# Optimization experiments

Measured on AMD Instinct MI355X. Metric: run time of the kernel, lower is better.

The kernel has to match this reference:

```python
import math
import jax, jax.numpy as jnp
import numpy as np

B, N, D = 32, 1025, 768        # batch, tokens (incl. CLS), backbone channels
C, CD, TD = 64, 128, 256       # num_clusters, cluster_dim, token_dim
REG = 0.1
SINKHORN_ITERS = 5


def setup_inputs() -> dict:
    key = jax.random.key(0)
    ks = jax.random.split(key, 9)
    inv = 1.0 / math.sqrt(D)
    return {
        "x": jax.random.normal(ks[0], (B, N, D), dtype=jnp.float32),
        "Wf": jax.random.normal(ks[1], (D, CD), dtype=jnp.float32) * inv,
        "bf": jnp.zeros((CD,), dtype=jnp.float32),
        "Ws": jax.random.normal(ks[2], (D, C), dtype=jnp.float32) * inv,
        "bs": jnp.zeros((C,), dtype=jnp.float32),
        "Wt": jax.random.normal(ks[3], (D, TD), dtype=jnp.float32) * inv,
        "bt": jnp.zeros((TD,), dtype=jnp.float32),
        "anchors": jax.random.normal(ks[4], (C, CD), dtype=jnp.float32) * 0.1,
        "dust_bin": jnp.array(1.0, dtype=jnp.float32),
        "sharpness": jnp.array(5.0, dtype=jnp.float32),
    }


def _sinkhorn_log(log_a, log_b, M, num_iters, reg):
    # log-domain Sinkhorn: M [B, C+1, Nt], log_a [B, C+1], log_b [B, Nt]
    M = M / reg
    u = jnp.zeros_like(log_a)
    v = jnp.zeros_like(log_b)
    for _ in range(num_iters):
        u = log_a - jax.nn.logsumexp(M + v[:, None, :], axis=2)
        v = log_b - jax.nn.logsumexp(M + u[:, :, None], axis=1)
    return M + u[:, :, None] + v[:, None, :]


def reference(x, Wf, bf, Ws, bs, Wt, bt, anchors, dust_bin, sharpness):
    Bx, Nx, _ = x.shape
    n_tok = Nx - 1
    nC = anchors.shape[0]

    t_global = x[:, 0]            # [B, D]
    fi = x[:, 1:]                 # [B, Nt, D]

    f = fi @ Wf + bf              # [B, Nt, CD]
    s = jnp.einsum('bnd,dc->bcn', fi, Ws) + bs[None, :, None]  # [B, C, Nt]
    s = s * sharpness

    dust = jnp.broadcast_to(dust_bin, (Bx, 1, n_tok))
    s_aug = jnp.concatenate([s, dust], axis=1)  # [B, C+1, Nt]

    log_b = jnp.full((Bx, n_tok), -math.log(n_tok), dtype=x.dtype)
    # n_tok (1024) > nC (64): marginals with dustbin absorbing excess mass
    log_a = jnp.concatenate([
        jnp.full((Bx, nC), -math.log(n_tok), dtype=x.dtype),
        jnp.full((Bx, 1), math.log(n_tok - nC) - math.log(n_tok), dtype=x.dtype),
    ], axis=1)

    log_P = _sinkhorn_log(log_a, log_b, s_aug, SINKHORN_ITERS, REG)
    p = jnp.exp(log_P)[:, :-1, :]  # [B, C, Nt], drop dustbin row

    # sum_n p[b,c,n] * (2*f[b,n,d] - anchors[c,d])  == GEMM + rank-1 correction
    v_agg = 2.0 * jnp.einsum('bcn,bnd->bcd', p, f) \
            - p.sum(axis=2)[:, :, None] * anchors[None]  # [B, C, CD]

    v_local = v_agg.reshape(Bx, -1)   # [B, C*CD]
    v_global = t_global @ Wt + bt     # [B, TD]
    f_out = jnp.concatenate([v_global, v_local], axis=-1)
    norm = jnp.maximum(jnp.linalg.norm(f_out, axis=-1, keepdims=True), 1e-12)
    return f_out / norm
```

## Files before the change

### kernel.cpp

```cpp
#include <hip/hip_runtime.h>

typedef unsigned short u16;
typedef __attribute__((ext_vector_type(8))) short bf16x8;
typedef __attribute__((ext_vector_type(8))) short s16x8;
typedef __attribute__((ext_vector_type(4))) float f32x4;
typedef __attribute__((ext_vector_type(4))) short s16x4;

#define OUTW 8448

static __device__ __forceinline__ float bf2f(u16 u) {
    union { unsigned int i; float f; } x; x.i = ((unsigned int)u) << 16; return x.f;
}
static __device__ __forceinline__ u16 f2bf(float f) {
    union { float f; unsigned int i; } x; x.f = f;
    unsigned int lsb = (x.i >> 16) & 1u;
    return (u16)((x.i + 0x7fffu + lsb) >> 16);
}
static __device__ __forceinline__ int kswz(int r, int c) {
    return c ^ (((r ^ (r >> 3)) & 7) << 3);
}

__global__ __launch_bounds__(256) void k_pre(
    const float* __restrict__ x, const float* __restrict__ Wf, const float* __restrict__ Ws,
    const float* __restrict__ Wt, u16* __restrict__ Bp, float* __restrict__ vg)
{
    const int bid = blockIdx.x, tid = threadIdx.x;
    if (bid < 12) {
        __shared__ float Wl[64][193];
        const int t = bid;
        #pragma unroll 4
        for (int i = 0; i < 32; ++i) {
            const int idx = i * 256 + tid, r = idx >> 7, c = idx & 127;
            Wl[r][c] = Wf[(size_t)(t * 64 + r) * 128 + c];
        }
        #pragma unroll 4
        for (int i = 0; i < 16; ++i) {
            const int idx = i * 256 + tid, r = idx >> 6, c = idx & 63;
            Wl[r][128 + c] = Ws[(size_t)(t * 64 + r) * 64 + c];
        }
        __syncthreads();
        #pragma unroll
        for (int i = 0; i < 6; ++i) {
            const int ch = i * 256 + tid, c = ch >> 3, j0 = (ch & 7) << 3;
            u16 pk[8];
            #pragma unroll
            for (int j = 0; j < 8; ++j) pk[j] = f2bf(Wl[j0 + j][c]);
            *(s16x8*)&Bp[((size_t)t * 192 + c) * 64 + j0] = *(const s16x8*)pk;
        }
    } else {
        const int blk = bid - 12;
        const int kc = blk >> 5, b = blk & 31, d = tid;
        const float* xr = x + (size_t)b * (1025 * 768) + kc * 96;
        const float* wp = Wt + (size_t)kc * 96 * 256 + d;
        float acc = 0.f;
        #pragma unroll 8
        for (int k = 0; k < 96; ++k) acc += xr[k] * wp[(size_t)k * 256];
        vg[(size_t)blk * 256 + d] = acc;
    }
}

__global__ __launch_bounds__(512, 4) void k_gemm1(
    const float* __restrict__ x, const u16* __restrict__ Bp,
    const float* __restrict__ bf_, const float* __restrict__ bs_, const float* __restrict__ sharp,
    u16* __restrict__ fT, float* __restrict__ sM)
{
    __shared__ u16 Asm[2][64][72];
    const int tid  = threadIdx.x;
    const int lane = tid & 63;
    const int w    = tid >> 6;
    const int wm   = w >> 2, wn = w & 3;
    const int b    = blockIdx.x >> 4;
    const int n0   = (blockIdx.x & 15) << 6;
    const float* Abase = x + ((size_t)b * 1025 + 1 + n0) * 768;

    const int arow = tid >> 3, ak0 = (tid & 7) << 3;
    const float* aptr = Abase + (size_t)arow * 768 + ak0;
    const int fk = (lane >> 4) << 3;
    const u16* bbase = Bp + (size_t)(wn * 48 + (lane & 15)) * 64 + fk;

    f32x4 acc[2][3] = {};
    float4 pa[2];
    bf16x8 bcur[6], bnxt[6];

    pa[0] = *(const float4*)(aptr);
    pa[1] = *(const float4*)(aptr + 4);
    #pragma unroll
    for (int nt = 0; nt < 3; ++nt)
        #pragma unroll
        for (int kk = 0; kk < 2; ++kk)
            bcur[nt * 2 + kk] = *(const bf16x8*)(bbase + nt * 1024 + kk * 32);
    {
        u16 t8[8];
        t8[0] = f2bf(pa[0].x); t8[1] = f2bf(pa[0].y); t8[2] = f2bf(pa[0].z); t8[3] = f2bf(pa[0].w);
        t8[4] = f2bf(pa[1].x); t8[5] = f2bf(pa[1].y); t8[6] = f2bf(pa[1].z); t8[7] = f2bf(pa[1].w);
        *(s16x8*)&Asm[0][arow][ak0] = *(const s16x8*)t8;
    }
    pa[0] = *(const float4*)(aptr + 64);
    pa[1] = *(const float4*)(aptr + 68);
    __syncthreads();

    for (int t = 0; t < 12; ++t) {
        const int cur = t & 1;
        if (t < 11) {
            const u16* bp1 = bbase + (size_t)(t + 1) * 12288;
            #pragma unroll
            for (int nt = 0; nt < 3; ++nt)
                #pragma unroll
                for (int kk = 0; kk < 2; ++kk)
                    bnxt[nt * 2 + kk] = *(const bf16x8*)(bp1 + nt * 1024 + kk * 32);
            u16 t8[8];
            t8[0] = f2bf(pa[0].x); t8[1] = f2bf(pa[0].y); t8[2] = f2bf(pa[0].z); t8[3] = f2bf(pa[0].w);
            t8[4] = f2bf(pa[1].x); t8[5] = f2bf(pa[1].y); t8[6] = f2bf(pa[1].z); t8[7] = f2bf(pa[1].w);
            *(s16x8*)&Asm[cur ^ 1][arow][ak0] = *(const s16x8*)t8;
        }
        if (t < 10) {
            const float* ap = aptr + (size_t)(t + 2) * 64;
            pa[0] = *(const float4*)(ap);
            pa[1] = *(const float4*)(ap + 4);
        }
        #pragma unroll
        for (int kk = 0; kk < 2; ++kk) {
            bf16x8 af[2];
            af[0] = *(const bf16x8*)&Asm[cur][wm * 32 + (lane & 15)][kk * 32 + fk];
            af[1] = *(const bf16x8*)&Asm[cur][wm * 32 + 16 + (lane & 15)][kk * 32 + fk];
            #pragma unroll
            for (int nt = 0; nt < 3; ++nt) {
                acc[0][nt] = __builtin_amdgcn_mfma_f32_16x16x32_bf16(af[0], bcur[nt * 2 + kk], acc[0][nt], 0, 0, 0);
                acc[1][nt] = __builtin_amdgcn_mfma_f32_16x16x32_bf16(af[1], bcur[nt * 2 + kk], acc[1][nt], 0, 0, 0);
            }
        }
        if (t < 11) {
            #pragma unroll
            for (int i = 0; i < 6; ++i) bcur[i] = bnxt[i];
        }
        __syncthreads();
    }

    const int rbase = (lane >> 4) << 2;
    const int cl = lane & 15;
    const float sc = sharp[0] * 10.0f;
    #pragma unroll
    for (int mt = 0; mt < 2; ++mt) {
        const int nbase = n0 + wm * 32 + mt * 16 + rbase;
        #pragma unroll
        for (int nt = 0; nt < 3; ++nt) {
            const int col16 = wn * 48 + nt * 16;
            const int c = col16 + cl;
            if (col16 < 128) {
                const float bias = bf_[c];
                u16 pk[4];
                #pragma unroll
                for (int r = 0; r < 4; ++r) pk[r] = f2bf(acc[mt][nt][r] + bias);
                *(s16x4*)&fT[((size_t)b * 128 + c) * 1024 + nbase] = *(const s16x4*)pk;
            } else {
                const int cm = c - 128;
                const float bias = bs_[cm];
                float4 v;
                v.x = (acc[mt][nt][0] + bias) * sc;
                v.y = (acc[mt][nt][1] + bias) * sc;
                v.z = (acc[mt][nt][2] + bias) * sc;
                v.w = (acc[mt][nt][3] + bias) * sc;
                *(float4*)&sM[((size_t)b * 64 + cm) * 1024 + nbase] = v;
            }
        }
    }
}

__global__ __launch_bounds__(1024, 1) void k_tail(
    const float* __restrict__ sM, const u16* __restrict__ fT,
    const float* __restrict__ vg, const float* __restrict__ bt,
    const float* __restrict__ anchors, float* __restrict__ out)
{
    __shared__ u16   Ksm[64][1024];
    __shared__ float betas[1024];
    __shared__ float alph[68];
    __shared__ float rsL[64];
    __shared__ float sred[16];
    const int b = blockIdx.x, tid = threadIdx.x, l = tid & 63, w = tid >> 6;
    const float* Mb = sM + (size_t)b * 64 * 1024;

    #pragma unroll
    for (int i = 0; i < 4; ++i) {
        const int c = w * 4 + i;
        float v[16];
        #pragma unroll
        for (int q = 0; q < 4; ++q)
            *(float4*)(v + q * 4) = *(const float4*)(Mb + (size_t)c * 1024 + l * 16 + q * 4);
        float mx = v[0];
        #pragma unroll
        for (int j = 1; j < 16; ++j) mx = fmaxf(mx, v[j]);
        #pragma unroll
        for (int off = 32; off > 0; off >>= 1) mx = fmaxf(mx, __shfl_xor(mx, off));
        u16 e[16];
        #pragma unroll
        for (int j = 0; j < 16; ++j) e[j] = f2bf(__expf(v[j] - mx));
        *(s16x8*)&Ksm[c][kswz(c, l * 16)]     = *(const s16x8*)(e);
        *(s16x8*)&Ksm[c][kswz(c, l * 16 + 8)] = *(const s16x8*)(e + 8);
    }
    betas[tid] = 1.0f;
    __syncthreads();

    const float a_c = 1.0f / 1024.0f, a_dust = 960.0f / 1024.0f, b_n = 1.0f / 1024.0f;
    const int r8  = (l & 7) * 8;
    const int cg  = w * 8 + (l >> 3);
    const int bwi = (cg & 63) + ((cg >> 6) << 9);

    for (int it = 0; it < 5; ++it) {
        float bb[16];
        #pragma unroll
        for (int j = 0; j < 2; ++j)
            #pragma unroll
            for (int m = 0; m < 8; ++m)
                bb[j * 8 + m] = betas[l + m * 64 + j * 512];
        float sb = 0.f;
        #pragma unroll
        for (int j = 0; j < 16; ++j) sb += bb[j];
        #pragma unroll
        for (int off = 32; off > 0; off >>= 1) sb += __shfl_xor(sb, off);
        #pragma unroll
        for (int i = 0; i < 4; ++i) {
            const int c = w * 4 + i;
            float s = 0.f;
            #pragma unroll
            for (int j = 0; j < 2; ++j) {
                const bf16x8 kr = *(const bf16x8*)&Ksm[c][kswz(c, 8 * l + 512 * j)];
                #pragma unroll
                for (int m = 0; m < 8; ++m) s += bf2f((u16)kr[m]) * bb[j * 8 + m];
            }
            #pragma unroll
            for (int off = 32; off > 0; off >>= 1) s += __shfl_xor(s, off);
            if (l == 0) alph[c] = a_c / s;
        }
        if (tid == 0) alph[64] = a_dust / sb;
        __syncthreads();
        f32x4 a0 = *(const f32x4*)&alph[r8];
        f32x4 a1 = *(const f32x4*)&alph[r8 + 4];
        const float ad = alph[64];
        float sc8[8] = {};
        #pragma unroll
        for (int i = 0; i < 8; ++i) {
            const bf16x8 kb = *(const bf16x8*)&Ksm[r8 + i][kswz(r8 + i, cg * 8)];
            const float av = (i < 4) ? a0[i] : a1[i - 4];
            #pragma unroll
            for (int m = 0; m < 8; ++m) sc8[m] += bf2f((u16)kb[m]) * av;
        }
        #pragma unroll
        for (int off = 1; off < 8; off <<= 1)
            #pragma unroll
            for (int m = 0; m < 8; ++m) sc8[m] += __shfl_xor(sc8[m], off);
        if ((l & 7) == 0) {
            #pragma unroll
            for (int m = 0; m < 8; ++m) betas[bwi + m * 64] = b_n / (sc8[m] + ad);
        }
        __syncthreads();
    }

    {
        float bb[16];
        #pragma unroll
        for (int j = 0; j < 2; ++j)
            #pragma unroll
            for (int m = 0; m < 8; ++m)
                bb[j * 8 + m] = betas[l + m * 64 + j * 512];
        #pragma unroll
        for (int i = 0; i < 4; ++i) {
            const int c = w * 4 + i;
            const float ac = alph[c];
            float s = 0.f;
            u16 pk[16];
            #pragma unroll
            for (int j = 0; j < 2; ++j) {
                const bf16x8 kr = *(const bf16x8*)&Ksm[c][kswz(c, 8 * l + 512 * j)];
                #pragma unroll
                for (int m = 0; m < 8; ++m) {
                    const float tv = bf2f((u16)kr[m]) * bb[j * 8 + m];
                    s += tv;
                    pk[j * 8 + m] = f2bf(ac * tv);
                }
            }
            #pragma unroll
            for (int off = 32; off > 0; off >>= 1) s += __shfl_xor(s, off);
            if (l == 0) rsL[c] = ac * s;
            *(s16x8*)&Ksm[c][kswz(c, 8 * l)]       = *(const s16x8*)(pk);
            *(s16x8*)&Ksm[c][kswz(c, 8 * l + 512)] = *(const s16x8*)(pk + 8);
        }
    }
    __syncthreads();

    const int mt = w & 3, ng = w >> 2;
    const int fk = (l >> 4) << 3;
    const int arow_ = mt * 16 + (l & 15);
    const u16* brow0 = fT + ((size_t)b * 128 + ng * 32 + (l & 15)) * 1024 + fk;
    const u16* brow1 = brow0 + 16 * 1024;
    f32x4 acc2[2] = {};
    #pragma unroll 4
    for (int ks = 0; ks < 32; ++ks) {
        const bf16x8 a  = *(const bf16x8*)&Ksm[arow_][kswz(arow_, ks * 32 + fk)];
        const bf16x8 b0 = *(const bf16x8*)(brow0 + ks * 32);
        const bf16x8 b1 = *(const bf16x8*)(brow1 + ks * 32);
        acc2[0] = __builtin_amdgcn_mfma_f32_16x16x32_bf16(a, b0, acc2[0], 0, 0, 0);
        acc2[1] = __builtin_amdgcn_mfma_f32_16x16x32_bf16(a, b1, acc2[1], 0, 0, 0);
    }

    float vgv = 0.f, ss = 0.f;
    if (tid < 256) {
        float v = bt[tid];
        #pragma unroll
        for (int kc = 0; kc < 8; ++kc) v += vg[(size_t)(kc * 32 + b) * 256 + tid];
        vgv = v; ss = v * v;
    }
    float vloc[2][4];
    #pragma unroll
    for (int nt = 0; nt < 2; ++nt) {
        const int d = ng * 32 + nt * 16 + (l & 15);
        #pragma unroll
        for (int r = 0; r < 4; ++r) {
            const int c = mt * 16 + ((l >> 4) << 2) + r;
            const float vv = 2.0f * acc2[nt][r] - rsL[c] * anchors[c * 128 + d];
            vloc[nt][r] = vv; ss += vv * vv;
        }
    }
    #pragma unroll
    for (int off = 32; off > 0; off >>= 1) ss += __shfl_xor(ss, off);
    if (l == 0) sred[w] = ss;
    __syncthreads();
    float tot = 0.f;
    #pragma unroll
    for (int i = 0; i < 16; ++i) tot += sred[i];
    const float inv = 1.0f / fmaxf(sqrtf(tot), 1e-12f);
    if (tid < 256) out[(size_t)b * OUTW + tid] = vgv * inv;
    #pragma unroll
    for (int nt = 0; nt < 2; ++nt) {
        const int d = ng * 32 + nt * 16 + (l & 15);
        #pragma unroll
        for (int r = 0; r < 4; ++r) {
            const int c = mt * 16 + ((l >> 4) << 2) + r;
            out[(size_t)b * OUTW + 256 + (size_t)c * 128 + d] = vloc[nt][r] * inv;
        }
    }
}

extern "C" void kernel_launch(void* const* d_in, const int* in_sizes, int n_in,
                              void* d_out, int out_size, void* d_ws, size_t ws_size,
                              hipStream_t stream)
{
    const float* x      = (const float*)d_in[0];
    const float* Wf     = (const float*)d_in[1];
    const float* bf_    = (const float*)d_in[2];
    const float* Ws     = (const float*)d_in[3];
    const float* bs_    = (const float*)d_in[4];
    const float* Wt     = (const float*)d_in[5];
    const float* bt     = (const float*)d_in[6];
    const float* anchors= (const float*)d_in[7];
    const float* sharp  = (const float*)d_in[9];

    char* ws = (char*)d_ws;
    u16*   fT = (u16*)(ws);
    float* sM = (float*)(ws + 8388608);
    u16*   Bp = (u16*)(ws + 16777216);
    float* vg = (float*)(ws + 17072128);
    float* out = (float*)d_out;

    k_pre  <<<dim3(268), 256,  0, stream>>>(x, Wf, Ws, Wt, Bp, vg);
    k_gemm1<<<dim3(512), 512,  0, stream>>>(x, Bp, bf_, bs_, sharp, fT, sM);
    k_tail <<<dim3(32),  1024, 0, stream>>>(sM, fT, vg, bt, anchors, out);
}
```

Before: 256.7 us.

## Halve gemm1 row tile to double block count; remap tail MFMA wave tiling

```diff
diff --git a/kernel.cpp b/kernel.cpp
--- a/kernel.cpp
+++ b/kernel.cpp
@@ -59,24 +59,23 @@
     }
 }
 
-__global__ __launch_bounds__(512, 4) void k_gemm1(
+__global__ __launch_bounds__(256, 4) void k_gemm1(
     const float* __restrict__ x, const u16* __restrict__ Bp,
     const float* __restrict__ bf_, const float* __restrict__ bs_, const float* __restrict__ sharp,
     u16* __restrict__ fT, float* __restrict__ sM)
 {
-    __shared__ u16 Asm[2][64][72];
+    __shared__ u16 Asm[2][32][72];
     const int tid  = threadIdx.x;
     const int lane = tid & 63;
     const int w    = tid >> 6;
-    const int wm   = w >> 2, wn = w & 3;
-    const int b    = blockIdx.x >> 4;
-    const int n0   = (blockIdx.x & 15) << 6;
+    const int b    = blockIdx.x >> 5;
+    const int n0   = (blockIdx.x & 31) << 5;
     const float* Abase = x + ((size_t)b * 1025 + 1 + n0) * 768;
 
     const int arow = tid >> 3, ak0 = (tid & 7) << 3;
     const float* aptr = Abase + (size_t)arow * 768 + ak0;
     const int fk = (lane >> 4) << 3;
-    const u16* bbase = Bp + (size_t)(wn * 48 + (lane & 15)) * 64 + fk;
+    const u16* bbase = Bp + (size_t)(w * 48 + (lane & 15)) * 64 + fk;
 
     f32x4 acc[2][3] = {};
     float4 pa[2];
@@ -121,8 +120,8 @@
         #pragma unroll
         for (int kk = 0; kk < 2; ++kk) {
             bf16x8 af[2];
-            af[0] = *(const bf16x8*)&Asm[cur][wm * 32 + (lane & 15)][kk * 32 + fk];
-            af[1] = *(const bf16x8*)&Asm[cur][wm * 32 + 16 + (lane & 15)][kk * 32 + fk];
+            af[0] = *(const bf16x8*)&Asm[cur][(lane & 15)][kk * 32 + fk];
+            af[1] = *(const bf16x8*)&Asm[cur][16 + (lane & 15)][kk * 32 + fk];
             #pragma unroll
             for (int nt = 0; nt < 3; ++nt) {
                 acc[0][nt] = __builtin_amdgcn_mfma_f32_16x16x32_bf16(af[0], bcur[nt * 2 + kk], acc[0][nt], 0, 0, 0);
@@ -141,10 +140,10 @@
     const float sc = sharp[0] * 10.0f;
     #pragma unroll
     for (int mt = 0; mt < 2; ++mt) {
-        const int nbase = n0 + wm * 32 + mt * 16 + rbase;
+        const int nbase = n0 + mt * 16 + rbase;
         #pragma unroll
         for (int nt = 0; nt < 3; ++nt) {
-            const int col16 = wn * 48 + nt * 16;
+            const int col16 = w * 48 + nt * 16;
             const int c = col16 + cl;
             if (col16 < 128) {
                 const float bias = bf_[c];
@@ -287,19 +286,19 @@
     }
     __syncthreads();
 
-    const int mt = w & 3, ng = w >> 2;
+    const int wng = w & 7, wmt = w >> 3;
     const int fk = (l >> 4) << 3;
-    const int arow_ = mt * 16 + (l & 15);
-    const u16* brow0 = fT + ((size_t)b * 128 + ng * 32 + (l & 15)) * 1024 + fk;
-    const u16* brow1 = brow0 + 16 * 1024;
+    const int ar0 = wmt * 32 + (l & 15);
+    const int ar1 = ar0 + 16;
+    const u16* brow = fT + ((size_t)b * 128 + wng * 16 + (l & 15)) * 1024 + fk;
     f32x4 acc2[2] = {};
     #pragma unroll 4
     for (int ks = 0; ks < 32; ++ks) {
-        const bf16x8 a  = *(const bf16x8*)&Ksm[arow_][kswz(arow_, ks * 32 + fk)];
-        const bf16x8 b0 = *(const bf16x8*)(brow0 + ks * 32);
-        const bf16x8 b1 = *(const bf16x8*)(brow1 + ks * 32);
-        acc2[0] = __builtin_amdgcn_mfma_f32_16x16x32_bf16(a, b0, acc2[0], 0, 0, 0);
-        acc2[1] = __builtin_amdgcn_mfma_f32_16x16x32_bf16(a, b1, acc2[1], 0, 0, 0);
+        const bf16x8 a0 = *(const bf16x8*)&Ksm[ar0][kswz(ar0, ks * 32 + fk)];
+        const bf16x8 a1 = *(const bf16x8*)&Ksm[ar1][kswz(ar1, ks * 32 + fk)];
+        const bf16x8 b0 = *(const bf16x8*)(brow + ks * 32);
+        acc2[0] = __builtin_amdgcn_mfma_f32_16x16x32_bf16(a0, b0, acc2[0], 0, 0, 0);
+        acc2[1] = __builtin_amdgcn_mfma_f32_16x16x32_bf16(a1, b0, acc2[1], 0, 0, 0);
     }
 
     float vgv = 0.f, ss = 0.f;
@@ -309,15 +308,15 @@
         for (int kc = 0; kc < 8; ++kc) v += vg[(size_t)(kc * 32 + b) * 256 + tid];
         vgv = v; ss = v * v;
     }
+    const int d5 = wng * 16 + (l & 15);
     float vloc[2][4];
     #pragma unroll
-    for (int nt = 0; nt < 2; ++nt) {
-        const int d = ng * 32 + nt * 16 + (l & 15);
+    for (int mt = 0; mt < 2; ++mt) {
         #pragma unroll
         for (int r = 0; r < 4; ++r) {
-            const int c = mt * 16 + ((l >> 4) << 2) + r;
-            const float vv = 2.0f * acc2[nt][r] - rsL[c] * anchors[c * 128 + d];
-            vloc[nt][r] = vv; ss += vv * vv;
+            const int c = wmt * 32 + mt * 16 + ((l >> 4) << 2) + r;
+            const float vv = 2.0f * acc2[mt][r] - rsL[c] * anchors[c * 128 + d5];
+            vloc[mt][r] = vv; ss += vv * vv;
         }
     }
     #pragma unroll
@@ -330,12 +329,11 @@
     const float inv = 1.0f / fmaxf(sqrtf(tot), 1e-12f);
     if (tid < 256) out[(size_t)b * OUTW + tid] = vgv * inv;
     #pragma unroll
-    for (int nt = 0; nt < 2; ++nt) {
-        const int d = ng * 32 + nt * 16 + (l & 15);
+    for (int mt = 0; mt < 2; ++mt) {
         #pragma unroll
         for (int r = 0; r < 4; ++r) {
-            const int c = mt * 16 + ((l >> 4) << 2) + r;
-            out[(size_t)b * OUTW + 256 + (size_t)c * 128 + d] = vloc[nt][r] * inv;
+            const int c = wmt * 32 + mt * 16 + ((l >> 4) << 2) + r;
+            out[(size_t)b * OUTW + 256 + (size_t)c * 128 + d5] = vloc[mt][r] * inv;
         }
     }
 }
@@ -361,7 +359,7 @@
     float* vg = (float*)(ws + 17072128);
     float* out = (float*)d_out;
 
-    k_pre  <<<dim3(268), 256,  0, stream>>>(x, Wf, Ws, Wt, Bp, vg);
-    k_gemm1<<<dim3(512), 512,  0, stream>>>(x, Bp, bf_, bs_, sharp, fT, sM);
-    k_tail <<<dim3(32),  1024, 0, stream>>>(sM, fT, vg, bt, anchors, out);
-}
+    k_pre  <<<dim3(268),  256,  0, stream>>>(x, Wf, Ws, Wt, Bp, vg);
+    k_gemm1<<<dim3(1024), 256,  0, stream>>>(x, Bp, bf_, bs_, sharp, fT, sM);
+    k_tail <<<dim3(32),   1024, 0, stream>>>(sM, fT, vg, bt, anchors, out);
+}
```

Measured after the change: 246.0 us. -4.1%, faster.
